# Optimization experiments

Hardware: AMD Instinct MI355X
Metric: run time of the kernel (lower is better)

The kernel has to match this reference:

```python
import jax, jax.numpy as jnp
import numpy as np

LATENT = 256
C = 512            # channels == window_size
STEP = C // 2      # 256
N_SAMPLES = 32768
N_FRAMES = N_SAMPLES // STEP   # 128
IMP = 4096         # impulse samples
B, E = 4, 64
EPS = 1e-8


def unit_norm(x, axis=-1):
    return x / (jnp.linalg.norm(x, axis=axis, keepdims=True) + EPS)


def hamming(n):
    # torch.hamming_window default (periodic=True)
    return (0.54 - 0.46 * jnp.cos(2.0 * jnp.pi * jnp.arange(n) / n)).astype(jnp.float32)


def layer_norm(x, g, b):
    mu = x.mean(-1, keepdims=True)
    var = x.var(-1, keepdims=True)
    return (x - mu) / jnp.sqrt(var + 1e-5) * g + b


def mlp(x, Ws, bs, g, bt):
    # LinearOutputStack: 3 hidden (linear -> LayerNorm -> leaky_relu) + output linear
    for j in range(3):
        x = x @ Ws[j] + bs[j]
        x = layer_norm(x, g[j], bt[j])
        x = jax.nn.leaky_relu(x, 0.2)
    return x @ Ws[3] + bs[3]


def _forward(embedding, impulse, W_def, b_def,
             Ws_imp, bs_imp, g_imp, bt_imp,
             Ws_lat, bs_lat, g_lat, bt_lat,
             Ws_out, bs_out, g_out, bt_out,
             W_w, b_w, W_b, b_b, W_l, b_l):
    Bq, Eq, _ = embedding.shape
    # shape deformations: latent -> (C, n_frames), unit-normed over channel dim
    deform = (embedding @ W_def + b_def).reshape(Bq, Eq, C, N_FRAMES)
    deform = unit_norm(deform, axis=2)
    deform = deform.transpose(0, 1, 3, 2)           # (B,E,T,C)
    weights = deform @ W_w + b_w                    # (B,E,T,C)
    biases = deform @ W_b + b_b                     # (B,E,T,C)
    leak = 0.1 + jax.nn.sigmoid(deform @ W_l + b_l) * 0.98  # (B,E,T,1)

    # window the impulse: frames of size C with hop STEP
    padded = jnp.pad(impulse, ((0, 0), (0, 0), (0, STEP)))
    starts = jnp.arange(IMP // STEP) * STEP
    idx = starts[:, None] + jnp.arange(C)[None, :]
    windowed = padded[..., idx]                     # (B,E,16,C)
    norms = jnp.linalg.norm(windowed, axis=-1, keepdims=True)
    emb = mlp(windowed, Ws_imp, bs_imp, g_imp, bt_imp)
    emb = unit_norm(emb) * norms                    # (B,E,16,C)
    # pad with zeros to n_frames: adding zero == original i < n_impulse_frames guard
    emb_pad = jnp.pad(emb, ((0, 0), (0, 0), (0, N_FRAMES - emb.shape[2]), (0, 0)))

    ham = hamming(C)

    xs = (weights.transpose(2, 0, 1, 3),
          biases.transpose(2, 0, 1, 3),
          leak.transpose(2, 0, 1, 3),
          emb_pad.transpose(2, 0, 1, 3))

    def step(h, x):
        w, b, lk, e = x
        h = h + e
        cn = jnp.linalg.norm(h, axis=-1, keepdims=True)
        h = h * w + b
        h = unit_norm(h) * cn
        ol = mlp(h, Ws_lat, bs_lat, g_lat, bt_lat)
        ol = unit_norm(ol) * (cn * lk)
        on = jnp.linalg.norm(ol, axis=-1, keepdims=True)
        h = h - ol
        h = unit_norm(h) * (cn - on)
        of = mlp(ol, Ws_out, bs_out, g_out, bt_out)
        of = of * ham
        of = unit_norm(of) * on
        return h, of

    h0 = jnp.zeros((Bq, Eq, C), dtype=embedding.dtype)
    _, frames = jax.lax.scan(step, h0, xs)          # (T,B,E,C)
    frames = frames.transpose(1, 2, 0, 3)           # (B,E,T,C)

    # overlap-add at hop STEP, trim to n_samples
    L = (N_FRAMES - 1) * STEP + C
    oa_idx = jnp.arange(N_FRAMES)[:, None] * STEP + jnp.arange(C)[None, :]
    out = jnp.zeros((Bq, Eq, L), dtype=embedding.dtype)
    out = out.at[:, :, oa_idx].add(frames)
    return out[..., :N_SAMPLES]


def setup_inputs() -> dict:
    key = jax.random.key(0)
    ks = jax.random.split(key, 24)
    s = 0.02
    d = {
        'embedding': jax.random.normal(ks[0], (B, E, LATENT), jnp.float32),
        'impulse': jax.random.normal(ks[1], (B, E, IMP), jnp.float32),
        'W_def': jax.random.normal(ks[2], (LATENT, C * N_FRAMES), jnp.float32) * s,
        'b_def': jnp.zeros((C * N_FRAMES,), jnp.float32),
        'W_w': jax.random.normal(ks[3], (C, C), jnp.float32) * s,
        'b_w': jnp.zeros((C,), jnp.float32),
        'W_b': jax.random.normal(ks[4], (C, C), jnp.float32) * s,
        'b_b': jnp.zeros((C,), jnp.float32),
        'W_l': jax.random.normal(ks[5], (C, 1), jnp.float32) * s,
        'b_l': jnp.zeros((1,), jnp.float32),
    }
    for name, k in (('imp', ks[6]), ('lat', ks[7]), ('out', ks[8])):
        d['Ws_' + name] = jax.random.normal(k, (4, C, C), jnp.float32) * s
        d['bs_' + name] = jnp.zeros((4, C), jnp.float32)
        d['g_' + name] = jnp.ones((3, C), jnp.float32)
        d['bt_' + name] = jnp.zeros((3, C), jnp.float32)
    return d


def reference(embedding, impulse, W_def, b_def,
              Ws_imp, bs_imp, g_imp, bt_imp,
              Ws_lat, bs_lat, g_lat, bt_lat,
              Ws_out, bs_out, g_out, bt_out,
              W_w, b_w, W_b, b_b, W_l, b_l):
    return _forward(embedding, impulse, W_def, b_def,
                    Ws_imp, bs_imp, g_imp, bt_imp,
                    Ws_lat, bs_lat, g_lat, bt_lat,
                    Ws_out, bs_out, g_out, bt_out,
                    W_w, b_w, W_b, b_b, W_l, b_l)
```

## Files before the change

### kernel.cpp

```cpp
#include <hip/hip_runtime.h>
#include <math.h>

#define NB 4
#define NE 64
#define BE 256
#define LAT 256
#define NC 512
#define NT 128
#define NDEF 65536
#define NIMP 4096
#define NF 16
#define EPSN 1e-8f
#define SPB 4
#define NSCAN 64
#define NSAMP 32768

typedef unsigned short ushort8 __attribute__((ext_vector_type(8)));
typedef short short8v __attribute__((ext_vector_type(8)));
typedef float f32x4 __attribute__((ext_vector_type(4)));

__device__ __forceinline__ unsigned short f2bf(float f) {
  const unsigned u = __float_as_uint(f);
  return (unsigned short)((u + 0x7FFFu + ((u >> 16) & 1u)) >> 16);
}

__device__ __forceinline__ void bar_nodrain() {
  asm volatile("s_waitcnt lgkmcnt(0)" ::: "memory");
  __builtin_amdgcn_s_barrier();
  __builtin_amdgcn_sched_barrier(0);
}

template <int NR>
__device__ __forceinline__ void blk_reduce1(const float* v, float* out,
                                            float* red) {
  const int tid = threadIdx.x, wave = tid >> 6, lane = tid & 63;
  float s[NR];
#pragma unroll
  for (int i = 0; i < NR; ++i) s[i] = v[i];
#pragma unroll
  for (int off = 32; off; off >>= 1) {
#pragma unroll
    for (int i = 0; i < NR; ++i) s[i] += __shfl_down(s[i], off);
  }
  if (lane == 0) {
#pragma unroll
    for (int i = 0; i < NR; ++i) red[wave * NR + i] = s[i];
  }
  bar_nodrain();
#pragma unroll
  for (int i = 0; i < NR; ++i) {
    float a = 0.f;
#pragma unroll
    for (int w = 0; w < 8; ++w) a += red[w * NR + i];
    out[i] = a;
  }
}

__global__ __launch_bounds__(64) void k_cvt(const float* __restrict__ W,
                                            unsigned short* __restrict__ Wmf) {
  const int lane = threadIdx.x;
  const int gg = blockIdx.x;
  const int p = gg & 3;
  const int kt = (gg >> 2) & 15;
  const int wv = (gg >> 6) & 7;
  const int layer = gg >> 9;
  const int col = wv * 64 + p * 16 + (lane & 15);
  const int k0 = kt * 32 + (lane >> 4) * 8;
  ushort8 o;
#pragma unroll
  for (int j = 0; j < 8; ++j)
    o[j] = f2bf(W[((size_t)layer * NC + k0 + j) * NC + col]);
  *reinterpret_cast<ushort8*>(Wmf + ((size_t)gg * 64 + lane) * 8) = o;
}

__global__ __launch_bounds__(256) void k_deform(
    const float* __restrict__ emb, const float* __restrict__ Wd,
    const float* __restrict__ bd, float* __restrict__ deform) {
  __shared__ float As[32][LAT];
  const int tid = threadIdx.x;
  const int c = blockIdx.x * 256 + tid;
  const int m0 = blockIdx.y * 32;
  for (int i = 0; i < 32; ++i) As[i][tid] = emb[(m0 + i) * LAT + tid];
  __syncthreads();
  float acc[32];
#pragma unroll
  for (int i = 0; i < 32; ++i) acc[i] = 0.f;
  for (int k = 0; k < LAT; k += 4) {
    const float w0 = Wd[(size_t)(k + 0) * NDEF + c];
    const float w1 = Wd[(size_t)(k + 1) * NDEF + c];
    const float w2 = Wd[(size_t)(k + 2) * NDEF + c];
    const float w3 = Wd[(size_t)(k + 3) * NDEF + c];
#pragma unroll
    for (int i = 0; i < 32; ++i) {
      const float4 a = *reinterpret_cast<const float4*>(&As[i][k]);
      acc[i] = fmaf(a.x, w0, acc[i]);
      acc[i] = fmaf(a.y, w1, acc[i]);
      acc[i] = fmaf(a.z, w2, acc[i]);
      acc[i] = fmaf(a.w, w3, acc[i]);
    }
  }
  const float bv = bd[c];
  for (int i = 0; i < 32; ++i)
    deform[(size_t)(m0 + i) * NDEF + c] = acc[i] + bv;
}

__global__ __launch_bounds__(512) void k_wb(
    const float* __restrict__ deform, const unsigned short* __restrict__ Wmf2,
    const float* __restrict__ bw, const float* __restrict__ bb,
    const float* __restrict__ Wl, const float* __restrict__ bl,
    float* __restrict__ weights, float* __restrict__ biases,
    float* __restrict__ leak) {
  __shared__ float xs[16][NC];
  __shared__ __align__(16) unsigned short A_lds[16 * NC];
  __shared__ float rno[16], lks[16];
  const int tid = threadIdx.x;
  const int wave = tid >> 6, lane = tid & 63;
  const int be = blockIdx.x >> 3;
  const int t0 = (blockIdx.x & 7) * 16;
  const float* dbase = deform + (size_t)be * NDEF;
  for (int i = 0; i < 16; ++i)
    xs[i][tid] = dbase[(size_t)tid * NT + t0 + i];
  __syncthreads();
  for (int f = wave; f < 16; f += 8) {
    float s = 0.f;
#pragma unroll
    for (int j = 0; j < 8; ++j) {
      const float v = xs[f][lane + 64 * j];
      s = fmaf(v, v, s);
    }
#pragma unroll
    for (int off = 32; off; off >>= 1) s += __shfl_down(s, off);
    if (lane == 0) rno[f] = sqrtf(s);
  }
  __syncthreads();
  {
    char* ab = (char*)A_lds;
#pragma unroll
    for (int i = 0; i < 16; ++i) {
      const float xv = xs[i][tid] / (rno[i] + EPSN);
      xs[i][tid] = xv;
      *(unsigned short*)(ab + i * 1024 + ((tid * 2) ^ ((i & 7) << 4))) =
          f2bf(xv);
    }
  }
  __syncthreads();
  for (int f = wave; f < 16; f += 8) {
    float s = 0.f;
#pragma unroll
    for (int j = 0; j < 8; ++j)
      s = fmaf(xs[f][lane + 64 * j], Wl[lane + 64 * j], s);
#pragma unroll
    for (int off = 32; off; off >>= 1) s += __shfl_down(s, off);
    if (lane == 0) lks[f] = s;
  }
  __syncthreads();
  if (tid < 16) {
    const float v = lks[tid] + bl[0];
    leak[(size_t)be * NT + t0 + tid] = 0.1f + 0.98f / (1.f + expf(-v));
  }
  const int arow = lane & 15;
  const int kgrp = lane >> 4;
  const int r0 = kgrp * 4;
  const int abase = arow * (NC * 2);
  const int axor = (arow & 7) << 4;
  const int akoff = kgrp * 16;
  float bwv[4], bbv[4];
#pragma unroll
  for (int p = 0; p < 4; ++p) {
    const int cp = wave * 64 + p * 16 + (lane & 15);
    bwv[p] = bw[cp];
    bbv[p] = bb[cp];
  }
  const unsigned short* wfrag = Wmf2 + (size_t)wave * 32768 + lane * 8;
  f32x4 accw[4], accb[4];
#pragma unroll
  for (int p = 0; p < 4; ++p) {
    accw[p] = (f32x4){0.f, 0.f, 0.f, 0.f};
    accb[p] = (f32x4){0.f, 0.f, 0.f, 0.f};
  }
#pragma unroll
  for (int kt = 0; kt < 16; ++kt) {
    const short8v a = *(const short8v*)((const char*)A_lds + abase +
                                        (((kt * 64) + akoff) ^ axor));
#pragma unroll
    for (int p = 0; p < 4; ++p) {
      const short8v b0 = *(const short8v*)(wfrag + (kt * 4 + p) * 512);
      accw[p] = __builtin_amdgcn_mfma_f32_16x16x32_bf16(a, b0, accw[p], 0, 0, 0);
      const short8v b1 =
          *(const short8v*)(wfrag + (size_t)262144 + (kt * 4 + p) * 512);
      accb[p] = __builtin_amdgcn_mfma_f32_16x16x32_bf16(a, b1, accb[p], 0, 0, 0);
    }
  }
#pragma unroll
  for (int q = 0; q < 4; ++q) {
    const int row = r0 + q;
#pragma unroll
    for (int p = 0; p < 4; ++p) {
      const int cp = wave * 64 + p * 16 + (lane & 15);
      const size_t o = ((size_t)be * NT + t0 + row) * NC + cp;
      weights[o] = accw[p][q] + bwv[p];
      biases[o] = accb[p][q] + bbv[p];
    }
  }
}

__device__ __forceinline__ void tile_gemm16(const float (*xs)[NC],
                                            const float* __restrict__ W,
                                            int tid, float acc[16]) {
#pragma unroll
  for (int i = 0; i < 16; ++i) acc[i] = 0.f;
  for (int k = 0; k < NC; k += 4) {
    const float w0 = W[(size_t)(k + 0) * NC + tid];
    const float w1 = W[(size_t)(k + 1) * NC + tid];
    const float w2 = W[(size_t)(k + 2) * NC + tid];
    const float w3 = W[(size_t)(k + 3) * NC + tid];
#pragma unroll
    for (int i = 0; i < 16; ++i) {
      const float4 a = *reinterpret_cast<const float4*>(&xs[i][k]);
      acc[i] = fmaf(a.x, w0, acc[i]);
      acc[i] = fmaf(a.y, w1, acc[i]);
      acc[i] = fmaf(a.z, w2, acc[i]);
      acc[i] = fmaf(a.w, w3, acc[i]);
    }
  }
}

__device__ __forceinline__ void ln_leaky16(float (*xs)[NC],
                                           const float* __restrict__ g,
                                           const float* __restrict__ bt,
                                           int layer, int tid, float* mu_s,
                                           float* rs_s) {
  const int wave = tid >> 6, lane = tid & 63;
  for (int f = wave; f < 16; f += 8) {
    float s = 0.f, s2 = 0.f;
#pragma unroll
    for (int j = 0; j < 8; ++j) {
      const float v = xs[f][lane + 64 * j];
      s += v;
      s2 = fmaf(v, v, s2);
    }
#pragma unroll
    for (int off = 32; off; off >>= 1) {
      s += __shfl_down(s, off);
      s2 += __shfl_down(s2, off);
    }
    if (lane == 0) {
      const float mu = s * (1.f / NC);
      mu_s[f] = mu;
      rs_s[f] = rsqrtf(s2 * (1.f / NC) - mu * mu + 1e-5f);
    }
  }
  __syncthreads();
  const float gv = g[layer * NC + tid], btv = bt[layer * NC + tid];
#pragma unroll
  for (int i = 0; i < 16; ++i) {
    const float y = (xs[i][tid] - mu_s[i]) * rs_s[i] * gv + btv;
    xs[i][tid] = y > 0.f ? y : 0.2f * y;
  }
  __syncthreads();
}

__global__ __launch_bounds__(512) void k_imp(
    const float* __restrict__ impulse, const float* __restrict__ Ws,
    const float* __restrict__ bs, const float* __restrict__ g,
    const float* __restrict__ bt, float* __restrict__ embo) {
  __shared__ float xs[16][NC];
  __shared__ float wno[16], mu_s[16], rs_s[16], ono[16];
  const int tid = threadIdx.x;
  const int wave = tid >> 6, lane = tid & 63;
  const int be = blockIdx.x;
  const float* ib = impulse + (size_t)be * NIMP;
  for (int f = 0; f < 16; ++f) {
    const int s = f * 256 + tid;
    xs[f][tid] = (s < NIMP) ? ib[s] : 0.f;
  }
  __syncthreads();
  for (int f = wave; f < 16; f += 8) {
    float s = 0.f;
#pragma unroll
    for (int j = 0; j < 8; ++j) {
      const float v = xs[f][lane + 64 * j];
      s = fmaf(v, v, s);
    }
#pragma unroll
    for (int off = 32; off; off >>= 1) s += __shfl_down(s, off);
    if (lane == 0) wno[f] = sqrtf(s);
  }
  __syncthreads();
  float acc[16];
  for (int layer = 0; layer < 4; ++layer) {
    tile_gemm16(xs, Ws + (size_t)layer * NC * NC, tid, acc);
    __syncthreads();
    const float bv = bs[layer * NC + tid];
#pragma unroll
    for (int i = 0; i < 16; ++i) xs[i][tid] = acc[i] + bv;
    __syncthreads();
    if (layer < 3) ln_leaky16(xs, g, bt, layer, tid, mu_s, rs_s);
  }
  for (int f = wave; f < 16; f += 8) {
    float s = 0.f;
#pragma unroll
    for (int j = 0; j < 8; ++j) {
      const float v = xs[f][lane + 64 * j];
      s = fmaf(v, v, s);
    }
#pragma unroll
    for (int off = 32; off; off >>= 1) s += __shfl_down(s, off);
    if (lane == 0) ono[f] = sqrtf(s);
  }
  __syncthreads();
  for (int f = 0; f < 16; ++f)
    embo[((size_t)be * NF + f) * NC + tid] =
        xs[f][tid] / (ono[f] + EPSN) * wno[f];
}

__global__ __launch_bounds__(512) void k_scan(
    const float* __restrict__ weights, const float* __restrict__ biases,
    const float* __restrict__ leak, const float* __restrict__ embw,
    const unsigned short* __restrict__ Wmf, const float* __restrict__ bs,
    const float* __restrict__ g, const float* __restrict__ bt,
    float* __restrict__ olb, float* __restrict__ onb) {
  __shared__ __align__(16) unsigned short A_lds[16 * NC];
  __shared__ __align__(16) unsigned short B_lds[8][4][2048];
  __shared__ float ol_lds[SPB][NC];
  __shared__ float redA[64];
  __shared__ float redB[32];
  __shared__ float st1[8][SPB], st2[8][SPB];
  __shared__ float lk_lds[SPB][NT];

  const int tid = threadIdx.x;
  const int wave = tid >> 6, lane = tid & 63;
  const int seq0 = blockIdx.x * SPB;

  {
    const int r = tid >> 7, tt = tid & 127;
    lk_lds[r][tt] = leak[(size_t)(seq0 + r) * NT + tt];
  }
  {
    unsigned* z = (unsigned*)(A_lds + SPB * NC);
    for (int i = tid; i < (16 - SPB) * NC / 2; i += 512) z[i] = 0u;
  }

  const int arow = lane & 15;
  const int kgrp = lane >> 4;
  const int abase = arow * (NC * 2);
  const int axor = (arow & 7) << 4;
  const int akoff = kgrp * 16;
  const bool crow = (kgrp == 0);

  float bsv[4][4], gv[3][4], btv[3][4];
#pragma unroll
  for (int p = 0; p < 4; ++p) {
    const int cp = wave * 64 + p * 16 + (lane & 15);
#pragma unroll
    for (int l = 0; l < 4; ++l) bsv[l][p] = bs[l * NC + cp];
#pragma unroll
    for (int l = 0; l < 3; ++l) {
      gv[l][p] = g[l * NC + cp];
      btv[l][p] = bt[l * NC + cp];
    }
  }
  const unsigned short* wfrag = Wmf + (size_t)wave * 32768 + lane * 8;

  auto issue_chunk = [&](int cc) {
    const int layer = cc >> 4, kt = cc & 15, slot = cc & 3;
#pragma unroll
    for (int p = 0; p < 4; ++p) {
      __builtin_amdgcn_global_load_lds(
          (const unsigned int*)(wfrag + (size_t)layer * 262144 +
                                (kt * 4 + p) * 512),
          (unsigned int*)&B_lds[wave][slot][p * 512], 16, 0, 0);
    }
  };

  float wpre[SPB], bpre[SPB], epre[SPB];
#pragma unroll
  for (int r = 0; r < SPB; ++r) {
    const size_t o = ((size_t)(seq0 + r) * NT) * NC + tid;
    wpre[r] = weights[o];
    bpre[r] = biases[o];
    epre[r] = embw[((size_t)(seq0 + r) * NF) * NC + tid];
  }

  __syncthreads();

  issue_chunk(0);
  issue_chunk(1);
  issue_chunk(2);

  float h[SPB], cn[SPB];
#pragma unroll
  for (int r = 0; r < SPB; ++r) { h[r] = 0.f; cn[r] = 0.f; }

#pragma unroll 1
  for (int t = 0; t < NT; ++t) {
    float hw[SPB];
    if (t < NF) {
#pragma unroll
      for (int r = 0; r < SPB; ++r) h[r] += epre[r];
      float v8[8], s8[8];
#pragma unroll
      for (int r = 0; r < SPB; ++r) {
        hw[r] = fmaf(h[r], wpre[r], bpre[r]);
        v8[r] = h[r] * h[r];
        v8[SPB + r] = hw[r] * hw[r];
      }
      if (t + 1 < NF) {
#pragma unroll
        for (int r = 0; r < SPB; ++r)
          epre[r] = embw[((size_t)(seq0 + r) * NF + t + 1) * NC + tid];
      }
      if (t + 1 < NT) {
#pragma unroll
        for (int r = 0; r < SPB; ++r) {
          const size_t o = ((size_t)(seq0 + r) * NT + t + 1) * NC + tid;
          wpre[r] = weights[o];
          bpre[r] = biases[o];
        }
      }
      blk_reduce1<8>(v8, s8, redA);
#pragma unroll
      for (int r = 0; r < SPB; ++r) {
        cn[r] = sqrtf(s8[r]);
        h[r] = hw[r] * (cn[r] / (sqrtf(s8[SPB + r]) + EPSN));
      }
    } else {
      float v4[SPB], s4[SPB];
#pragma unroll
      for (int r = 0; r < SPB; ++r) {
        hw[r] = fmaf(h[r], wpre[r], bpre[r]);
        v4[r] = hw[r] * hw[r];
      }
      if (t + 1 < NT) {
#pragma unroll
        for (int r = 0; r < SPB; ++r) {
          const size_t o = ((size_t)(seq0 + r) * NT + t + 1) * NC + tid;
          wpre[r] = weights[o];
          bpre[r] = biases[o];
        }
      }
      blk_reduce1<SPB>(v4, s4, redA);
#pragma unroll
      for (int r = 0; r < SPB; ++r)
        h[r] = hw[r] * (cn[r] / (sqrtf(s4[r]) + EPSN));
    }
    {
      char* ab = (char*)A_lds;
#pragma unroll
      for (int r = 0; r < SPB; ++r)
        *(unsigned short*)(ab + r * 1024 + ((tid * 2) ^ ((r & 7) << 4))) =
            f2bf(h[r]);
    }
    bar_nodrain();

#pragma unroll 1
    for (int layer = 0; layer < 4; ++layer) {
      f32x4 acc[4];
#pragma unroll
      for (int p = 0; p < 4; ++p) acc[p] = (f32x4){0.f, 0.f, 0.f, 0.f};
#pragma unroll
      for (int kt = 0; kt < 16; ++kt) {
        asm volatile("s_waitcnt vmcnt(8)" ::: "memory");
        const short8v a = *(const short8v*)((const char*)A_lds + abase +
                                            (((kt * 64) + akoff) ^ axor));
        const int slot = kt & 3;
#pragma unroll
        for (int p = 0; p < 4; ++p) {
          const short8v b =
              *(const short8v*)((const char*)&B_lds[wave][slot][0] + p * 1024 +
                                lane * 16);
          acc[p] =
              __builtin_amdgcn_mfma_f32_16x16x32_bf16(a, b, acc[p], 0, 0, 0);
        }
        issue_chunk((layer * 16 + kt + 3) & 63);
      }

      if (layer < 3) {
        float s1[SPB], s2[SPB];
#pragma unroll
        for (int q = 0; q < SPB; ++q) { s1[q] = 0.f; s2[q] = 0.f; }
#pragma unroll
        for (int p = 0; p < 4; ++p) {
#pragma unroll
          for (int q = 0; q < SPB; ++q) {
            const float y = acc[p][q] + bsv[layer][p];
            acc[p][q] = y;
            s1[q] += y;
            s2[q] = fmaf(y, y, s2[q]);
          }
        }
#pragma unroll
        for (int off = 1; off < 16; off <<= 1) {
#pragma unroll
          for (int q = 0; q < SPB; ++q) {
            s1[q] += __shfl_xor(s1[q], off);
            s2[q] += __shfl_xor(s2[q], off);
          }
        }
        if (lane == 0) {
#pragma unroll
          for (int q = 0; q < SPB; ++q) {
            st1[wave][q] = s1[q];
            st2[wave][q] = s2[q];
          }
        }
        bar_nodrain();
        float mu[SPB], rs[SPB];
#pragma unroll
        for (int q = 0; q < SPB; ++q) {
          float a1 = 0.f, a2 = 0.f;
#pragma unroll
          for (int w = 0; w < 8; ++w) {
            a1 += st1[w][q];
            a2 += st2[w][q];
          }
          mu[q] = a1 * (1.f / NC);
          rs[q] = rsqrtf(a2 * (1.f / NC) - mu[q] * mu[q] + 1e-5f);
        }
        if (crow) {
          char* ab = (char*)A_lds;
#pragma unroll
          for (int q = 0; q < SPB; ++q) {
#pragma unroll
            for (int p = 0; p < 4; ++p) {
              float y = (acc[p][q] - mu[q]) * rs[q] * gv[layer][p] +
                        btv[layer][p];
              y = y > 0.f ? y : 0.2f * y;
              const int cp = wave * 64 + p * 16 + (lane & 15);
              *(unsigned short*)(ab + q * 1024 +
                                 ((cp * 2) ^ ((q & 7) << 4))) = f2bf(y);
            }
          }
        }
        bar_nodrain();
      } else {
        float s2[SPB];
#pragma unroll
        for (int q = 0; q < SPB; ++q) s2[q] = 0.f;
#pragma unroll
        for (int p = 0; p < 4; ++p) {
#pragma unroll
          for (int q = 0; q < SPB; ++q) {
            const float y = acc[p][q] + bsv[3][p];
            acc[p][q] = y;
            s2[q] = fmaf(y, y, s2[q]);
          }
        }
#pragma unroll
        for (int off = 1; off < 16; off <<= 1) {
#pragma unroll
          for (int q = 0; q < SPB; ++q) s2[q] += __shfl_xor(s2[q], off);
        }
        if (lane == 0) {
#pragma unroll
          for (int q = 0; q < SPB; ++q) st2[wave][q] = s2[q];
        }
        if (crow) {
#pragma unroll
          for (int q = 0; q < SPB; ++q) {
#pragma unroll
            for (int p = 0; p < 4; ++p)
              ol_lds[q][wave * 64 + p * 16 + (lane & 15)] = acc[p][q];
          }
        }
        bar_nodrain();
        float sc[SPB], on[SPB];
#pragma unroll
        for (int r = 0; r < SPB; ++r) {
          float a2 = 0.f;
#pragma unroll
          for (int w = 0; w < 8; ++w) a2 += st2[w][r];
          const float no = sqrtf(a2);
          sc[r] = cn[r] * lk_lds[r][t] / (no + EPSN);
          on[r] = no * sc[r];
        }
        if (tid < SPB) onb[(size_t)(seq0 + tid) * NT + t] = on[tid];
        float v4[SPB], s4[SPB];
#pragma unroll
        for (int r = 0; r < SPB; ++r) {
          const float olv = ol_lds[r][tid] * sc[r];
          olb[((size_t)(seq0 + r) * NT + t) * NC + tid] = olv;
          h[r] -= olv;
          v4[r] = h[r] * h[r];
        }
        blk_reduce1<SPB>(v4, s4, redB);
#pragma unroll
        for (int r = 0; r < SPB; ++r) {
          h[r] *= (cn[r] - on[r]) / (sqrtf(s4[r]) + EPSN);
          cn[r] = fabsf(cn[r] - on[r]);
        }
      }
    }
  }
}

__global__ __launch_bounds__(1024) void k_zero(float* __restrict__ out) {
  out[(size_t)blockIdx.x * 1024 + threadIdx.x] = 0.f;
}

__global__ __launch_bounds__(512) void k_out(
    const float* __restrict__ olb, const float* __restrict__ onb,
    const unsigned short* __restrict__ Wmf, const float* __restrict__ bs,
    const float* __restrict__ g, const float* __restrict__ bt,
    float* __restrict__ out) {
  __shared__ __align__(16) unsigned short A_lds[16 * NC];
  __shared__ float st1[8][16], st2[8][16];
  __shared__ float on_l[16];
  const int tid = threadIdx.x;
  const int wave = tid >> 6, lane = tid & 63;
  const int m0 = blockIdx.x * 16;
  const int arow = lane & 15;
  const int kgrp = lane >> 4;
  const int r0 = kgrp * 4;
  const int abase = arow * (NC * 2);
  const int axor = (arow & 7) << 4;
  const int akoff = kgrp * 16;

  float bsv[4][4], gv[3][4], btv[3][4], hamv[4];
#pragma unroll
  for (int p = 0; p < 4; ++p) {
    const int cp = wave * 64 + p * 16 + (lane & 15);
#pragma unroll
    for (int l = 0; l < 4; ++l) bsv[l][p] = bs[l * NC + cp];
#pragma unroll
    for (int l = 0; l < 3; ++l) {
      gv[l][p] = g[l * NC + cp];
      btv[l][p] = bt[l * NC + cp];
    }
    hamv[p] =
        0.54f - 0.46f * cosf(6.283185307179586f * (float)cp / (float)NC);
  }
  if (tid < 16) on_l[tid] = onb[m0 + tid];
  {
    char* ab = (char*)A_lds;
    for (int i = 0; i < 16; ++i) {
      const float v = olb[(size_t)(m0 + i) * NC + tid];
      *(unsigned short*)(ab + i * 1024 + ((tid * 2) ^ ((i & 7) << 4))) =
          f2bf(v);
    }
  }
  __syncthreads();

  const unsigned short* wfrag = Wmf + (size_t)wave * 32768 + lane * 8;

#pragma unroll 1
  for (int layer = 0; layer < 4; ++layer) {
    f32x4 acc[4];
#pragma unroll
    for (int p = 0; p < 4; ++p) acc[p] = (f32x4){0.f, 0.f, 0.f, 0.f};
#pragma unroll
    for (int kt = 0; kt < 16; ++kt) {
      const short8v a = *(const short8v*)((const char*)A_lds + abase +
                                          (((kt * 64) + akoff) ^ axor));
#pragma unroll
      for (int p = 0; p < 4; ++p) {
        const short8v b = *(const short8v*)(wfrag + (size_t)layer * 262144 +
                                            (kt * 4 + p) * 512);
        acc[p] = __builtin_amdgcn_mfma_f32_16x16x32_bf16(a, b, acc[p], 0, 0, 0);
      }
    }
    if (layer < 3) {
      float s1[4], s2[4];
#pragma unroll
      for (int q = 0; q < 4; ++q) { s1[q] = 0.f; s2[q] = 0.f; }
#pragma unroll
      for (int p = 0; p < 4; ++p) {
#pragma unroll
        for (int q = 0; q < 4; ++q) {
          const float y = acc[p][q] + bsv[layer][p];
          acc[p][q] = y;
          s1[q] += y;
          s2[q] = fmaf(y, y, s2[q]);
        }
      }
#pragma unroll
      for (int off = 1; off < 16; off <<= 1) {
#pragma unroll
        for (int q = 0; q < 4; ++q) {
          s1[q] += __shfl_xor(s1[q], off);
          s2[q] += __shfl_xor(s2[q], off);
        }
      }
      if ((lane & 15) == 0) {
#pragma unroll
        for (int q = 0; q < 4; ++q) {
          st1[wave][r0 + q] = s1[q];
          st2[wave][r0 + q] = s2[q];
        }
      }
      __syncthreads();
      char* ab = (char*)A_lds;
#pragma unroll
      for (int q = 0; q < 4; ++q) {
        const int row = r0 + q;
        float a1 = 0.f, a2 = 0.f;
#pragma unroll
        for (int w = 0; w < 8; ++w) {
          a1 += st1[w][row];
          a2 += st2[w][row];
        }
        const float mu = a1 * (1.f / NC);
        const float rs = rsqrtf(a2 * (1.f / NC) - mu * mu + 1e-5f);
#pragma unroll
        for (int p = 0; p < 4; ++p) {
          float y = (acc[p][q] - mu) * rs * gv[layer][p] + btv[layer][p];
          y = y > 0.f ? y : 0.2f * y;
          const int cp = wave * 64 + p * 16 + (lane & 15);
          *(unsigned short*)(ab + row * 1024 +
                             ((cp * 2) ^ ((row & 7) << 4))) = f2bf(y);
        }
      }
      __syncthreads();
    } else {
      float s2[4];
#pragma unroll
      for (int q = 0; q < 4; ++q) s2[q] = 0.f;
#pragma unroll
      for (int p = 0; p < 4; ++p) {
#pragma unroll
        for (int q = 0; q < 4; ++q) {
          float y = (acc[p][q] + bsv[3][p]) * hamv[p];
          acc[p][q] = y;
          s2[q] = fmaf(y, y, s2[q]);
        }
      }
#pragma unroll
      for (int off = 1; off < 16; off <<= 1) {
#pragma unroll
        for (int q = 0; q < 4; ++q) s2[q] += __shfl_xor(s2[q], off);
      }
      if ((lane & 15) == 0) {
#pragma unroll
        for (int q = 0; q < 4; ++q) st2[wave][r0 + q] = s2[q];
      }
      __syncthreads();
#pragma unroll
      for (int q = 0; q < 4; ++q) {
        const int row = r0 + q;
        const int gr = m0 + row;
        const int be = gr >> 7;
        const int tt = gr & 127;
        float a2 = 0.f;
#pragma unroll
        for (int w = 0; w < 8; ++w) a2 += st2[w][row];
        const float inv = on_l[row] / (sqrtf(a2) + EPSN);
#pragma unroll
        for (int p = 0; p < 4; ++p) {
          const int cp = wave * 64 + p * 16 + (lane & 15);
          const int s = tt * 256 + cp;
          if (s < NSAMP)
            atomicAdd(&out[(size_t)be * NSAMP + s], acc[p][q] * inv);
        }
      }
    }
  }
}

extern "C" void kernel_launch(void* const* d_in, const int* in_sizes, int n_in,
                              void* d_out, int out_size, void* d_ws,
                              size_t ws_size, hipStream_t stream) {
  const float* embedding = (const float*)d_in[0];
  const float* impulse = (const float*)d_in[1];
  const float* W_def = (const float*)d_in[2];
  const float* b_def = (const float*)d_in[3];
  const float* W_w = (const float*)d_in[4];
  const float* b_w = (const float*)d_in[5];
  const float* W_b = (const float*)d_in[6];
  const float* b_b = (const float*)d_in[7];
  const float* W_l = (const float*)d_in[8];
  const float* b_l = (const float*)d_in[9];
  const float* Ws_imp = (const float*)d_in[10];
  const float* bs_imp = (const float*)d_in[11];
  const float* g_imp = (const float*)d_in[12];
  const float* bt_imp = (const float*)d_in[13];
  const float* Ws_lat = (const float*)d_in[14];
  const float* bs_lat = (const float*)d_in[15];
  const float* g_lat = (const float*)d_in[16];
  const float* bt_lat = (const float*)d_in[17];
  const float* Ws_out = (const float*)d_in[18];
  const float* bs_out = (const float*)d_in[19];
  const float* g_out = (const float*)d_in[20];
  const float* bt_out = (const float*)d_in[21];
  float* out = (float*)d_out;

  float* ws = (float*)d_ws;
  float* deform = ws;
  float* weights = deform + 16777216;
  float* biases = weights + 16777216;
  float* leakb = biases + 16777216;
  float* embw = leakb + 32768;
  float* onb = embw + 2097152;
  unsigned short* wmf = (unsigned short*)(onb + 32768);
  unsigned short* wmf_out = wmf + 1048576;
  unsigned short* wmf_wb = wmf_out + 1048576;
  float* olb = deform;

  k_cvt<<<2048, 64, 0, stream>>>(Ws_lat, wmf);
  k_cvt<<<2048, 64, 0, stream>>>(Ws_out, wmf_out);
  k_cvt<<<512, 64, 0, stream>>>(W_w, wmf_wb);
  k_cvt<<<512, 64, 0, stream>>>(W_b, wmf_wb + 262144);
  k_deform<<<dim3(256, 8), 256, 0, stream>>>(embedding, W_def, b_def, deform);
  k_wb<<<2048, 512, 0, stream>>>(deform, wmf_wb, b_w, b_b, W_l, b_l,
                                 weights, biases, leakb);
  k_imp<<<256, 512, 0, stream>>>(impulse, Ws_imp, bs_imp, g_imp, bt_imp, embw);
  k_zero<<<(BE * NSAMP) / 1024, 1024, 0, stream>>>(out);
  k_scan<<<NSCAN, 512, 0, stream>>>(weights, biases, leakb, embw, wmf, bs_lat,
                                    g_lat, bt_lat, olb, onb);
  k_out<<<2048, 512, 0, stream>>>(olb, onb, wmf_out, bs_out, g_out, bt_out,
                                  out);
}
```

Baseline: 4.312 ms.

## Move deform projection to bf16 MFMA with pre-converted fragment weights

Replaces the scalar fp32 FMA GEMM for the latent-to-deform projection with bf16 MFMA 16x16x32 instructions. A new conversion kernel first packs W_def into bf16 fragment layout, placed in the weights buffer before k_wb overwrites it. The activation tile goes to swizzled LDS to avoid bank conflicts. The k_wb transposed load is reorganized and its LDS row padded to reduce bank conflicts. This trades fp32 precision for bf16 and adds a conversion pass over the 64 MB weight every call.

```diff
diff --git a/kernel.cpp b/kernel.cpp
--- a/kernel.cpp
+++ b/kernel.cpp
@@ -73,35 +73,77 @@
   *reinterpret_cast<ushort8*>(Wmf + ((size_t)gg * 64 + lane) * 8) = o;
 }
 
-__global__ __launch_bounds__(256) void k_deform(
-    const float* __restrict__ emb, const float* __restrict__ Wd,
+__global__ __launch_bounds__(64) void k_cvt_def(
+    const float* __restrict__ W, unsigned short* __restrict__ Wd) {
+  const int lane = threadIdx.x;
+  const int gg = blockIdx.x;
+  const int p = gg & 3;
+  const int kt = (gg >> 2) & 7;
+  const int wv = (gg >> 5) & 7;
+  const int nb = gg >> 8;
+  const int col = nb * 512 + wv * 64 + p * 16 + (lane & 15);
+  const int k0 = kt * 32 + (lane >> 4) * 8;
+  ushort8 o;
+#pragma unroll
+  for (int j = 0; j < 8; ++j)
+    o[j] = f2bf(W[(size_t)(k0 + j) * NDEF + col]);
+  *reinterpret_cast<ushort8*>(Wd + ((size_t)gg * 64 + lane) * 8) = o;
+}
+
+__global__ __launch_bounds__(512) void k_deform(
+    const float* __restrict__ emb, const unsigned short* __restrict__ Wd,
     const float* __restrict__ bd, float* __restrict__ deform) {
-  __shared__ float As[32][LAT];
+  __shared__ __align__(16) unsigned short A_lds[16 * LAT];
   const int tid = threadIdx.x;
-  const int c = blockIdx.x * 256 + tid;
-  const int m0 = blockIdx.y * 32;
-  for (int i = 0; i < 32; ++i) As[i][tid] = emb[(m0 + i) * LAT + tid];
-  __syncthreads();
-  float acc[32];
-#pragma unroll
-  for (int i = 0; i < 32; ++i) acc[i] = 0.f;
-  for (int k = 0; k < LAT; k += 4) {
-    const float w0 = Wd[(size_t)(k + 0) * NDEF + c];
-    const float w1 = Wd[(size_t)(k + 1) * NDEF + c];
-    const float w2 = Wd[(size_t)(k + 2) * NDEF + c];
-    const float w3 = Wd[(size_t)(k + 3) * NDEF + c];
-#pragma unroll
-    for (int i = 0; i < 32; ++i) {
-      const float4 a = *reinterpret_cast<const float4*>(&As[i][k]);
-      acc[i] = fmaf(a.x, w0, acc[i]);
-      acc[i] = fmaf(a.y, w1, acc[i]);
-      acc[i] = fmaf(a.z, w2, acc[i]);
-      acc[i] = fmaf(a.w, w3, acc[i]);
-    }
-  }
-  const float bv = bd[c];
-  for (int i = 0; i < 32; ++i)
-    deform[(size_t)(m0 + i) * NDEF + c] = acc[i] + bv;
+  const int wave = tid >> 6, lane = tid & 63;
+  const int nb = blockIdx.x;
+  const int m0 = blockIdx.y * 16;
+  {
+    char* ab = (char*)A_lds;
+#pragma unroll
+    for (int rep = 0; rep < 8; ++rep) {
+      const int idx = rep * 512 + tid;
+      const int row = idx >> 8;
+      const int k = idx & 255;
+      *(unsigned short*)(ab + row * 512 + ((k * 2) ^ ((row & 7) << 4))) =
+          f2bf(emb[(size_t)(m0 + row) * LAT + k]);
+    }
+  }
+  __syncthreads();
+  const int arow = lane & 15;
+  const int kgrp = lane >> 4;
+  const int r0 = kgrp * 4;
+  const int abase = arow * 512;
+  const int axor = (arow & 7) << 4;
+  const int akoff = kgrp * 16;
+  float bdv[4];
+#pragma unroll
+  for (int p = 0; p < 4; ++p)
+    bdv[p] = bd[nb * 512 + wave * 64 + p * 16 + (lane & 15)];
+  const unsigned short* wfrag =
+      Wd + (size_t)(nb * 8 + wave) * 16384 + lane * 8;
+  f32x4 acc[4];
+#pragma unroll
+  for (int p = 0; p < 4; ++p) acc[p] = (f32x4){0.f, 0.f, 0.f, 0.f};
+#pragma unroll
+  for (int kt = 0; kt < 8; ++kt) {
+    const short8v a = *(const short8v*)((const char*)A_lds + abase +
+                                        (((kt * 64) + akoff) ^ axor));
+#pragma unroll
+    for (int p = 0; p < 4; ++p) {
+      const short8v b = *(const short8v*)(wfrag + (kt * 4 + p) * 512);
+      acc[p] = __builtin_amdgcn_mfma_f32_16x16x32_bf16(a, b, acc[p], 0, 0, 0);
+    }
+  }
+#pragma unroll
+  for (int q = 0; q < 4; ++q) {
+    const int row = r0 + q;
+#pragma unroll
+    for (int p = 0; p < 4; ++p) {
+      const int col = nb * 512 + wave * 64 + p * 16 + (lane & 15);
+      deform[(size_t)(m0 + row) * NDEF + col] = acc[p][q] + bdv[p];
+    }
+  }
 }
 
 __global__ __launch_bounds__(512) void k_wb(
@@ -110,7 +152,7 @@
     const float* __restrict__ Wl, const float* __restrict__ bl,
     float* __restrict__ weights, float* __restrict__ biases,
     float* __restrict__ leak) {
-  __shared__ float xs[16][NC];
+  __shared__ float xs[16][NC + 1];
   __shared__ __align__(16) unsigned short A_lds[16 * NC];
   __shared__ float rno[16], lks[16];
   const int tid = threadIdx.x;
@@ -118,8 +160,13 @@
   const int be = blockIdx.x >> 3;
   const int t0 = (blockIdx.x & 7) * 16;
   const float* dbase = deform + (size_t)be * NDEF;
-  for (int i = 0; i < 16; ++i)
-    xs[i][tid] = dbase[(size_t)tid * NT + t0 + i];
+#pragma unroll
+  for (int rep = 0; rep < 16; ++rep) {
+    const int idx = rep * 512 + tid;
+    const int c = idx >> 4;
+    const int f = idx & 15;
+    xs[f][c] = dbase[(size_t)c * NT + t0 + f];
+  }
   __syncthreads();
   for (int f = wave; f < 16; f += 8) {
     float s = 0.f;
@@ -793,13 +840,16 @@
   unsigned short* wmf = (unsigned short*)(onb + 32768);
   unsigned short* wmf_out = wmf + 1048576;
   unsigned short* wmf_wb = wmf_out + 1048576;
+  unsigned short* wmf_def = (unsigned short*)weights;
   float* olb = deform;
 
   k_cvt<<<2048, 64, 0, stream>>>(Ws_lat, wmf);
   k_cvt<<<2048, 64, 0, stream>>>(Ws_out, wmf_out);
   k_cvt<<<512, 64, 0, stream>>>(W_w, wmf_wb);
   k_cvt<<<512, 64, 0, stream>>>(W_b, wmf_wb + 262144);
-  k_deform<<<dim3(256, 8), 256, 0, stream>>>(embedding, W_def, b_def, deform);
+  k_cvt_def<<<32768, 64, 0, stream>>>(W_def, wmf_def);
+  k_deform<<<dim3(128, 16), 512, 0, stream>>>(embedding, wmf_def, b_def,
+                                              deform);
   k_wb<<<2048, 512, 0, stream>>>(deform, wmf_wb, b_w, b_b, W_l, b_l,
                                  weights, biases, leakb);
   k_imp<<<256, 512, 0, stream>>>(impulse, Ws_imp, bs_imp, g_imp, bt_imp, embw);
```

Measured after the change: 4.170 ms. -3.3%, faster.
